# Kernel optimization log

Measured on AMD Instinct MI355X. Metric: run time of the kernel, lower is better.

## Reference

```python
import jax, jax.numpy as jnp
import numpy as np

SEGMENT_LENGTHS = (768, 1536, 3072, 6144, 12288)
DILATED_RATIOS = (1, 2, 4, 8, 16)
NUM_HEADS = 12
NEG_INF = -1e9


def _layer_norm(x, g, b, eps=1e-5):
    mu = jnp.mean(x, axis=-1, keepdims=True)
    var = jnp.mean((x - mu) ** 2, axis=-1, keepdims=True)
    return (x - mu) * jax.lax.rsqrt(var + eps) * g + b


def _dilated_branch(q, k, v, w, r):
    # q,k,v: (B, L, H, Dh); segment length w, dilation ratio r (w % r == 0)
    B, L, H, Dh = q.shape
    Lp = -(-L // w) * w
    n, m = Lp // w, w // r
    gsz = -(-H // r)  # head-group size (heads padded up to a multiple of r in LongNet)
    offs = jnp.arange(H) // gsz  # per-head token offset within each r-block
    oh = jax.nn.one_hot(offs, r, dtype=q.dtype)  # (H, r)

    def gather(t):
        t = jnp.pad(t, ((0, 0), (0, Lp - L), (0, 0), (0, 0)))
        t = t.reshape(B, n, m, r, H, Dh)  # segments of w = m blocks of r
        return jnp.einsum('bnmrhd,hr->bnmhd', t, oh)  # each head picks its offset

    qi, ki, vi = gather(q), gather(k), gather(v)
    s = jnp.einsum('bnihd,bnjhd->bnhij', qi * (Dh ** -0.5), ki)  # (B,n,H,m,m)
    lse = jax.scipy.special.logsumexp(s, axis=-1)  # (B,n,H,m)
    o = jnp.einsum('bnhij,bnjhd->bnihd', jax.nn.softmax(s, axis=-1), vi)
    # scatter back to dense token positions; uncovered slots get 0 / -inf lse
    o_full = jnp.einsum('bnmhd,hr->bnmrhd', o, oh).reshape(B, Lp, H, Dh)
    lse = jnp.transpose(lse, (0, 1, 3, 2))  # (B,n,m,H)
    lse_full = jnp.where(oh.T[None, None, None] > 0, lse[:, :, :, None, :], NEG_INF)
    lse_full = lse_full.reshape(B, Lp, H)
    return o_full[:, :L], lse_full[:, :L]


def _dilated_attention(q, k, v):
    outs, lses = [], []
    for w, r in zip(SEGMENT_LENGTHS, DILATED_RATIOS):
        o, l = _dilated_branch(q, k, v, w, r)
        outs.append(o)
        lses.append(l)
    lse = jnp.stack(lses)  # (n_branch, B, L, H)
    wts = jnp.exp(lse - lse.max(0))
    wts = wts / wts.sum(0)  # softmax-combine branches by their lse (LongNet recombination)
    return (jnp.stack(outs) * wts[..., None]).sum(0)  # (B, L, H, Dh)


def _forward(x, patch_w, patch_b, cls_token, pos_embed,
             ln1_g, ln1_b, wq, bq, wk, bk, wv, bv, wo, bo,
             ln2_g, ln2_b, w1, b1, w2, b2, normf_g, normf_b, head_w, head_b):
    B, Cin, D, Hs, Ws = x.shape
    E = patch_w.shape[0]
    pd, ph, pw = patch_w.shape[2], patch_w.shape[3], patch_w.shape[4]
    # non-overlapping 3D patch embed (Conv3d with stride == kernel)
    xp = x.reshape(B, Cin, D // pd, pd, Hs // ph, ph, Ws // pw, pw)
    tok = jnp.einsum('bcxpyqzr,ecpqr->bxyze', xp, patch_w).reshape(B, -1, E) + patch_b
    tok = tok + pos_embed[:, 1:]
    cls = cls_token + pos_embed[:, :1]
    h = jnp.concatenate([jnp.broadcast_to(cls, (B, 1, E)), tok], axis=1)
    L = h.shape[1]
    Dh = E // NUM_HEADS
    depth = wq.shape[0]
    for i in range(depth):  # pre-LN transformer layers with LongNet dilated attention
        hn = _layer_norm(h, ln1_g[i], ln1_b[i])
        q = (hn @ wq[i] + bq[i]).reshape(B, L, NUM_HEADS, Dh)
        k = (hn @ wk[i] + bk[i]).reshape(B, L, NUM_HEADS, Dh)
        v = (hn @ wv[i] + bv[i]).reshape(B, L, NUM_HEADS, Dh)
        a = _dilated_attention(q, k, v).reshape(B, L, E)
        h = h + a @ wo[i] + bo[i]
        hn = _layer_norm(h, ln2_g[i], ln2_b[i])
        h = h + jax.nn.gelu(hn @ w1[i] + b1[i], approximate=False) @ w2[i] + b2[i]
    h = _layer_norm(h, normf_g, normf_b)
    return h[:, 0] @ head_w + head_b  # (B, num_classes)


def setup_inputs() -> dict:
    key = jax.random.key(0)
    ks = jax.random.split(key, 12)
    B, E, depth, ncls = 2, 768, 2, 1000
    D, Hs, Ws = 48, 256, 256
    N = (D // 4) * (Hs // 16) * (Ws // 16)  # 3072 patches
    f32 = jnp.float32
    s = 0.02
    return {
        'x': jax.random.normal(ks[0], (B, 1, D, Hs, Ws), f32),
        'patch_w': jax.random.normal(ks[1], (E, 1, 4, 16, 16), f32) * s,
        'patch_b': jnp.zeros((E,), f32),
        'cls_token': jax.random.normal(ks[2], (1, 1, E), f32) * s,
        'pos_embed': jax.random.normal(ks[3], (1, N + 1, E), f32) * s,
        'ln1_g': jnp.ones((depth, E), f32),
        'ln1_b': jnp.zeros((depth, E), f32),
        'wq': jax.random.normal(ks[4], (depth, E, E), f32) * s,
        'bq': jnp.zeros((depth, E), f32),
        'wk': jax.random.normal(ks[5], (depth, E, E), f32) * s,
        'bk': jnp.zeros((depth, E), f32),
        'wv': jax.random.normal(ks[6], (depth, E, E), f32) * s,
        'bv': jnp.zeros((depth, E), f32),
        'wo': jax.random.normal(ks[7], (depth, E, E), f32) * s,
        'bo': jnp.zeros((depth, E), f32),
        'ln2_g': jnp.ones((depth, E), f32),
        'ln2_b': jnp.zeros((depth, E), f32),
        'w1': jax.random.normal(ks[8], (depth, E, 4 * E), f32) * s,
        'b1': jnp.zeros((depth, 4 * E), f32),
        'w2': jax.random.normal(ks[9], (depth, 4 * E, E), f32) * s,
        'b2': jnp.zeros((depth, E), f32),
        'normf_g': jnp.ones((E,), f32),
        'normf_b': jnp.zeros((E,), f32),
        'head_w': jax.random.normal(ks[10], (E, ncls), f32) * s,
        'head_b': jnp.zeros((ncls,), f32),
    }


def reference(x, patch_w, patch_b, cls_token, pos_embed,
              ln1_g, ln1_b, wq, bq, wk, bk, wv, bv, wo, bo,
              ln2_g, ln2_b, w1, b1, w2, b2, normf_g, normf_b, head_w, head_b):
    return _forward(x, patch_w, patch_b, cls_token, pos_embed,
                    ln1_g, ln1_b, wq, bq, wk, bk, wv, bv, wo, bo,
                    ln2_g, ln2_b, w1, b1, w2, b2, normf_g, normf_b, head_w, head_b)
```

## Files before the change

kernel.cpp:

```cpp
#include <hip/hip_runtime.h>
#include <math.h>

#define TOK_L 3073
#define EMB 768
#define NH 12
#define DH 64
#define BATCH 2
#define QKVS 2304
#define HSZ ((size_t)BATCH * TOK_L * EMB)
#define MHC ((size_t)BATCH * TOK_L * NH)

typedef __bf16 bf16;
typedef __bf16 v8bf __attribute__((ext_vector_type(8)));
typedef __bf16 v4bf __attribute__((ext_vector_type(4)));
typedef float  v4f  __attribute__((ext_vector_type(4)));
typedef unsigned int v4u __attribute__((ext_vector_type(4)));

__device__ __forceinline__ v8bf zero8() {
    v8bf v;
    #pragma unroll
    for (int i = 0; i < 8; i++) v[i] = (bf16)0.f;
    return v;
}
__device__ __forceinline__ v4f zero4() {
    v4f v; v[0] = 0.f; v[1] = 0.f; v[2] = 0.f; v[3] = 0.f; return v;
}
__device__ __forceinline__ float gelu_f(float x) {
    return 0.5f * x * (1.0f + erff(x * 0.70710678118654752f));
}
__device__ __forceinline__ void gload16(const bf16* g, bf16* l) {
    __builtin_amdgcn_global_load_lds(
        (const __attribute__((address_space(1))) void*)g,
        (__attribute__((address_space(3))) void*)l, 16, 0, 0);
}
__device__ __forceinline__ v8bf lds_read128(const bf16* p) {
    v8bf r;
    asm volatile("ds_read_b128 %0, %1"
        : "=v"(r)
        : "v"((const __attribute__((address_space(3))) bf16*)p));
    return r;
}

__device__ __forceinline__ void convT_tile(const float* __restrict__ src,
                                           bf16* __restrict__ dst,
                                           int K, int N, int tx, int ty)
{
    __shared__ float t[32][33];
    int n0 = tx * 32, k0 = ty * 32;
    int r = threadIdx.x >> 3, c4 = (threadIdx.x & 7) * 4;
    float4 v = *(const float4*)(src + (size_t)(k0 + r) * N + n0 + c4);
    t[r][c4 + 0] = v.x; t[r][c4 + 1] = v.y; t[r][c4 + 2] = v.z; t[r][c4 + 3] = v.w;
    __syncthreads();
    v4bf o;
    o[0] = (bf16)t[c4 + 0][r]; o[1] = (bf16)t[c4 + 1][r];
    o[2] = (bf16)t[c4 + 2][r]; o[3] = (bf16)t[c4 + 3][r];
    *(v4bf*)(dst + (size_t)(n0 + r) * K + k0 + c4) = o;
}

__global__ __launch_bounds__(256) void prep_weights(
    const float* __restrict__ wq, const float* __restrict__ wk,
    const float* __restrict__ wv, const float* __restrict__ wo,
    const float* __restrict__ w1, const float* __restrict__ w2,
    const float* __restrict__ patch_w,
    bf16* __restrict__ qkv_t0, bf16* __restrict__ wo_t0,
    bf16* __restrict__ w1_t, bf16* __restrict__ w2_t, bf16* __restrict__ pw_b)
{
    int bid = blockIdx.x;
    if (bid >= 13824) {
        int i = ((bid - 13824) * 256 + threadIdx.x) * 4;
        float4 v = *(const float4*)(patch_w + i);
        v4bf o; o[0] = (bf16)v.x; o[1] = (bf16)v.y; o[2] = (bf16)v.z; o[3] = (bf16)v.w;
        *(v4bf*)(pw_b + i) = o;
        return;
    }
    int layer = bid / 6912, t = bid % 6912;
    if (t < 1728) {
        int m = t / 576, tt = t % 576;
        const float* src = (m == 0 ? wq : m == 1 ? wk : wv) + (size_t)layer * 589824;
        bf16* dst = qkv_t0 + (size_t)layer * QKVS * 768 + (size_t)m * 589824;
        convT_tile(src, dst, 768, 768, tt % 24, tt / 24);
    } else if (t < 2304) {
        int tt = t - 1728;
        convT_tile(wo + (size_t)layer * 589824, wo_t0 + (size_t)layer * 589824,
                   768, 768, tt % 24, tt / 24);
    } else if (t < 4608) {
        int tt = t - 2304;
        convT_tile(w1 + (size_t)layer * 2359296, w1_t + (size_t)layer * 2359296,
                   768, 3072, tt % 96, tt / 96);
    } else {
        int tt = t - 4608;
        convT_tile(w2 + (size_t)layer * 2359296, w2_t + (size_t)layer * 2359296,
                   3072, 768, tt % 24, tt / 24);
    }
}

__global__ __launch_bounds__(256) void prep_small(const float* __restrict__ bq,
    const float* __restrict__ bk, const float* __restrict__ bv, float* __restrict__ d,
    const float* __restrict__ cls, const float* __restrict__ pos, float* __restrict__ h)
{
    int i = blockIdx.x * 256 + threadIdx.x;
    if (i < 2 * QKVS) {
        int layer = i / QKVS, j = i % QKVS;
        const float* s = (j < 768) ? bq : (j < 1536) ? bk : bv;
        d[i] = s[(size_t)layer * 768 + (j & 767)];
    }
    if (i < 2 * 768) {
        int b = i / 768, e = i % 768;
        h[(size_t)b * TOK_L * EMB + e] = cls[e] + pos[e];
    }
}

__global__ __launch_bounds__(256) void gather_patches(const float* __restrict__ x,
                                                      bf16* __restrict__ Xp) {
    int p = blockIdx.x;
    int b = p / 3072, pp = p % 3072;
    int px = pp >> 8, py = (pp >> 4) & 15, pz = pp & 15;
    for (int k = threadIdx.x; k < 1024; k += 256) {
        int pd = k >> 8, ph = (k >> 4) & 15, pw = k & 15;
        size_t src = ((size_t)(b * 48 + px * 4 + pd)) * 65536
                   + (size_t)(py * 16 + ph) * 256 + (size_t)(pz * 16 + pw);
        Xp[(size_t)p * 1024 + k] = (bf16)x[src];
    }
}

__device__ __forceinline__ void remap_tile(int NX, int MY, int G, int& xo, int& yo)
{
    int id = blockIdx.x + NX * blockIdx.y;
    int nwg = NX * MY;
    int xcd = id & 7, j = id >> 3;
    int q = nwg >> 3, r = nwg & 7;
    int n = xcd * q + (xcd < r ? xcd : r) + j;
    int full = MY / G;
    int bpg = NX * G;
    int nf = full * bpg;
    if (n < nf) {
        int gi = n / bpg, w = n - gi * bpg;
        int xi = w / G;
        xo = xi; yo = gi * G + (w - xi * G);
    } else {
        int t = MY - full * G;
        int w = n - nf;
        int xi = w / t;
        xo = xi; yo = full * G + (w - xi * t);
    }
}

__global__ __launch_bounds__(512, 2) void gemm256(
    const bf16* __restrict__ A, const bf16* __restrict__ Bt,
    const float* __restrict__ bias, bf16* __restrict__ Cb,
    int M, int N, int K, int dogelu, int G)
{
    __shared__ bf16 AB[65536];
    const int tid = threadIdx.x;
    const int lane = tid & 63, wid = tid >> 6;
    const int ln15 = lane & 15, q4 = lane >> 4;
    int xo, yo;
    remap_tile(gridDim.x, gridDim.y, G, xo, yo);
    const int m0 = yo * 256, n0 = xo * 256;
    const int wm = (wid & 1) * 128, wn = (wid >> 1) * 64;
    const int srow = wid * 8 + (lane >> 3);
    const int schunk = ((lane & 7) ^ ((lane >> 3) & 7)) * 8;
    const int NT = K >> 6;

    auto stageA = [&](int t, int h) {
        const int slot = (2 * t + h) & 3;
        bf16* dstb = AB + slot * 8192 + wid * 512;
        const int k0 = t << 6;
        #pragma unroll
        for (int i = 0; i < 2; i++) {
            int gm = m0 + h * 128 + i * 64 + srow; if (gm >= M) gm = M - 1;
            gload16(A + (size_t)gm * K + k0 + schunk, dstb + i * 4096);
        }
    };
    auto stageB = [&](int t, int h) {
        const int slot = (2 * t + h) & 3;
        bf16* dstb = AB + 32768 + slot * 8192 + wid * 512;
        const int k0 = t << 6;
        #pragma unroll
        for (int i = 0; i < 2; i++) {
            int gn = n0 + h * 128 + i * 64 + srow;
            gload16(Bt + (size_t)gn * K + k0 + schunk, dstb + i * 4096);
        }
    };
    auto rdA = [&](int kt, int mt, int ks) -> v8bf {
        int R = wm + mt * 16 + ln15;
        int slot = (2 * kt + (R >> 7)) & 3;
        int r7 = R & 127;
        return lds_read128(AB + slot * 8192 + r7 * 64 + ((ks * 4 + q4) ^ (r7 & 7)) * 8);
    };
    auto rdB = [&](int kt, int nt, int ks) -> v8bf {
        int C = wn + nt * 16 + ln15;
        int slot = (2 * kt + (C >> 7)) & 3;
        int c7 = C & 127;
        return lds_read128(AB + 32768 + slot * 8192 + c7 * 64 + ((ks * 4 + q4) ^ (c7 & 7)) * 8);
    };

    v4f acc[8][4];
    #pragma unroll
    for (int i = 0; i < 8; i++)
        #pragma unroll
        for (int j = 0; j < 4; j++) acc[i][j] = zero4();

    stageA(0, 0); stageA(0, 1); stageB(0, 0); stageB(0, 1);
    if (NT > 1) { stageA(1, 0); stageA(1, 1); }

    v8bf af[8][2], bfr[4][2];
    for (int kt = 0; kt < NT; kt++) {
        if (kt + 1 < NT) {
            stageB(kt + 1, 0);
            asm volatile("s_waitcnt vmcnt(6)" ::: "memory");
        } else {
            asm volatile("s_waitcnt vmcnt(0)" ::: "memory");
        }
        __builtin_amdgcn_sched_barrier(0);
        __builtin_amdgcn_s_barrier();
        __builtin_amdgcn_sched_barrier(0);
        #pragma unroll
        for (int mt = 0; mt < 4; mt++) { af[mt][0] = rdA(kt, mt, 0); af[mt][1] = rdA(kt, mt, 1); }
        #pragma unroll
        for (int nt = 0; nt < 2; nt++) { bfr[nt][0] = rdB(kt, nt, 0); bfr[nt][1] = rdB(kt, nt, 1); }
        asm volatile("s_waitcnt lgkmcnt(0)" ::: "memory");
        __builtin_amdgcn_sched_barrier(0);
        __builtin_amdgcn_s_setprio(1);
        #pragma unroll
        for (int mt = 0; mt < 4; mt++)
            #pragma unroll
            for (int nt = 0; nt < 2; nt++)
                #pragma unroll
                for (int ks = 0; ks < 2; ks++)
                    acc[mt][nt] = __builtin_amdgcn_mfma_f32_16x16x32_bf16(af[mt][ks], bfr[nt][ks], acc[mt][nt], 0, 0, 0);
        __builtin_amdgcn_s_setprio(0);
        __builtin_amdgcn_s_barrier();
        #pragma unroll
        for (int mt = 4; mt < 8; mt++) { af[mt][0] = rdA(kt, mt, 0); af[mt][1] = rdA(kt, mt, 1); }
        #pragma unroll
        for (int nt = 2; nt < 4; nt++) { bfr[nt][0] = rdB(kt, nt, 0); bfr[nt][1] = rdB(kt, nt, 1); }
        if (kt + 1 < NT) stageB(kt + 1, 1);
        __builtin_amdgcn_s_barrier();
        asm volatile("s_waitcnt lgkmcnt(0)" ::: "memory");
        __builtin_amdgcn_sched_barrier(0);
        __builtin_amdgcn_s_setprio(1);
        #pragma unroll
        for (int mt = 0; mt < 4; mt++)
            #pragma unroll
            for (int nt = 2; nt < 4; nt++)
                #pragma unroll
                for (int ks = 0; ks < 2; ks++)
                    acc[mt][nt] = __builtin_amdgcn_mfma_f32_16x16x32_bf16(af[mt][ks], bfr[nt][ks], acc[mt][nt], 0, 0, 0);
        __builtin_amdgcn_s_setprio(0);
        __builtin_amdgcn_s_barrier();
        if (kt + 2 < NT) stageA(kt + 2, 0);
        __builtin_amdgcn_s_barrier();
        __builtin_amdgcn_sched_barrier(0);
        __builtin_amdgcn_s_setprio(1);
        #pragma unroll
        for (int mt = 4; mt < 8; mt++)
            #pragma unroll
            for (int nt = 2; nt < 4; nt++)
                #pragma unroll
                for (int ks = 0; ks < 2; ks++)
                    acc[mt][nt] = __builtin_amdgcn_mfma_f32_16x16x32_bf16(af[mt][ks], bfr[nt][ks], acc[mt][nt], 0, 0, 0);
        __builtin_amdgcn_s_setprio(0);
        __builtin_amdgcn_s_barrier();
        if (kt + 2 < NT) stageA(kt + 2, 1);
        __builtin_amdgcn_s_barrier();
        __builtin_amdgcn_sched_barrier(0);
        __builtin_amdgcn_s_setprio(1);
        #pragma unroll
        for (int mt = 4; mt < 8; mt++)
            #pragma unroll
            for (int nt = 0; nt < 2; nt++)
                #pragma unroll
                for (int ks = 0; ks < 2; ks++)
                    acc[mt][nt] = __builtin_amdgcn_mfma_f32_16x16x32_bf16(af[mt][ks], bfr[nt][ks], acc[mt][nt], 0, 0, 0);
        __builtin_amdgcn_s_setprio(0);
        __builtin_amdgcn_s_barrier();
    }

    #pragma unroll
    for (int mt = 0; mt < 8; mt++) {
        #pragma unroll
        for (int nt = 0; nt < 4; nt++) {
            #pragma unroll
            for (int g = 0; g < 4; g++) {
                int row = m0 + wm + mt * 16 + q4 * 4 + g;
                if (row >= M) continue;
                int col = n0 + wn + nt * 16 + ln15;
                float v = acc[mt][nt][g] + bias[col];
                if (dogelu) v = gelu_f(v);
                Cb[(size_t)row * N + col] = (bf16)v;
            }
        }
    }
}

template<int BN>
__global__ __launch_bounds__(256) void gemm_bf16(
    const bf16* __restrict__ A, const bf16* __restrict__ Bt,
    const float* __restrict__ bias, float* __restrict__ Cf,
    bf16* __restrict__ Cb, int M, int N, int K, int flags,
    const float* __restrict__ pos, int G)
{
    __shared__ bf16 As[3][128 * 32];
    __shared__ bf16 Bs[3][BN * 32];
    const int tid = threadIdx.x;
    const int lane = tid & 63, wid = tid >> 6;
    const int ln15 = lane & 15, q4 = lane >> 4;
    int xo, yo;
    remap_tile(gridDim.x, gridDim.y, G, xo, yo);
    const int m0 = yo * 128, n0 = xo * BN;
    const int wm = (wid & 1) * 64, wn = (wid >> 1) * (BN / 2);
    const int srow = lane >> 2;
    const int schunk = (lane & 3) * 8;
    const int NF = BN / 32;

    v4f acc[4][NF];
    #pragma unroll
    for (int i = 0; i < 4; i++)
        #pragma unroll
        for (int j = 0; j < NF; j++) acc[i][j] = zero4();

    const int NT = K >> 5;
    auto stage = [&](int kt, int bi) {
        const int k0 = kt << 5;
        #pragma unroll
        for (int i = 0; i < 2; i++) {
            int rg = wid * 32 + i * 16;
            int gm = m0 + rg + srow; if (gm >= M) gm = M - 1;
            gload16(A + (size_t)gm * K + k0 + schunk, &As[bi][rg * 32]);
        }
        if (BN == 128) {
            #pragma unroll
            for (int i = 0; i < 2; i++) {
                int rg = wid * 32 + i * 16;
                gload16(Bt + (size_t)(n0 + rg + srow) * K + k0 + schunk, &Bs[bi][rg * 32]);
            }
        } else {
            int rg = wid * 16;
            gload16(Bt + (size_t)(n0 + rg + srow) * K + k0 + schunk, &Bs[bi][rg * 32]);
        }
    };

    stage(0, 0);
    if (NT > 1) stage(1, 1);

    int cur = 0;
    for (int kt = 0; kt < NT; kt++) {
        int nx2 = cur + 2; if (nx2 >= 3) nx2 -= 3;
        if (kt + 2 < NT) {
            stage(kt + 2, nx2);
            if (BN == 128) asm volatile("s_waitcnt vmcnt(8)" ::: "memory");
            else           asm volatile("s_waitcnt vmcnt(6)" ::: "memory");
        } else if (kt + 1 < NT) {
            if (BN == 128) asm volatile("s_waitcnt vmcnt(4)" ::: "memory");
            else           asm volatile("s_waitcnt vmcnt(3)" ::: "memory");
        } else {
            asm volatile("s_waitcnt vmcnt(0)" ::: "memory");
        }
        __builtin_amdgcn_sched_barrier(0);
        __builtin_amdgcn_s_barrier();

        v8bf af[4], bfr[NF];
        #pragma unroll
        for (int mt = 0; mt < 4; mt++)
            af[mt] = *(const v8bf*)(&As[cur][(wm + mt * 16 + ln15) * 32 + q4 * 8]);
        #pragma unroll
        for (int nt = 0; nt < NF; nt++)
            bfr[nt] = *(const v8bf*)(&Bs[cur][(wn + nt * 16 + ln15) * 32 + q4 * 8]);
        #pragma unroll
        for (int mt = 0; mt < 4; mt++)
            #pragma unroll
            for (int nt = 0; nt < NF; nt++)
                acc[mt][nt] = __builtin_amdgcn_mfma_f32_16x16x32_bf16(af[mt], bfr[nt], acc[mt][nt], 0, 0, 0);
        __builtin_amdgcn_s_barrier();
        cur = cur + 1 == 3 ? 0 : cur + 1;
    }
    #pragma unroll
    for (int mt = 0; mt < 4; mt++) {
        #pragma unroll
        for (int nt = 0; nt < NF; nt++) {
            #pragma unroll
            for (int g = 0; g < 4; g++) {
                int row = m0 + wm + mt * 16 + q4 * 4 + g;
                if (row >= M) continue;
                int col = n0 + wn + nt * 16 + ln15;
                float v = acc[mt][nt][g] + bias[col];
                if (flags & 2) v = gelu_f(v);
                size_t crow;
                if (flags & 4) {
                    int rowp = row % 3072;
                    crow = (size_t)(row + row / 3072 + 1);
                    v += pos[(size_t)(rowp + 1) * EMB + col];
                } else crow = (size_t)row;
                size_t ci = crow * (size_t)N + col;
                if (flags & 8) Cb[ci] = (bf16)v;
                else { if (flags & 1) v += Cf[ci]; Cf[ci] = v; }
            }
        }
    }
}

__global__ __launch_bounds__(256) void layernorm_kernel(
    const float* __restrict__ x, const float* __restrict__ g,
    const float* __restrict__ bb, bf16* __restrict__ y, int nrows)
{
    int row = blockIdx.x;
    if (row >= nrows) return;
    int tid = threadIdx.x;
    const float* xr = x + (size_t)row * EMB;
    float v0 = xr[tid], v1 = xr[tid + 256], v2 = xr[tid + 512];
    __shared__ float red[256];
    red[tid] = v0 + v1 + v2;
    __syncthreads();
    for (int o = 128; o > 0; o >>= 1) { if (tid < o) red[tid] += red[tid + o]; __syncthreads(); }
    float mu = red[0] * (1.f / 768.f);
    __syncthreads();
    float d0 = v0 - mu, d1 = v1 - mu, d2 = v2 - mu;
    red[tid] = d0 * d0 + d1 * d1 + d2 * d2;
    __syncthreads();
    for (int o = 128; o > 0; o >>= 1) { if (tid < o) red[tid] += red[tid + o]; __syncthreads(); }
    float rs = rsqrtf(red[0] * (1.f / 768.f) + 1e-5f);
    bf16* yr = y + (size_t)row * EMB;
    yr[tid]       = (bf16)(d0 * rs * g[tid]       + bb[tid]);
    yr[tid + 256] = (bf16)(d1 * rs * g[tid + 256] + bb[tid + 256]);
    yr[tid + 512] = (bf16)(d2 * rs * g[tid + 512] + bb[tid + 512]);
}

__global__ __launch_bounds__(256) void pack_vt(const bf16* __restrict__ qkv,
                                               bf16* __restrict__ Vt)
{
    __shared__ bf16 t[64 * 65];
    int yy = blockIdx.y;
    int br, seg;
    if (yy < 5)       { br = 0; seg = yy; }
    else if (yy < 8)  { br = 1; seg = yy - 5; }
    else if (yy < 10) { br = 2; seg = yy - 8; }
    else if (yy == 10){ br = 3; seg = 0; }
    else              { br = 4; seg = 0; }
    const int r = 1 << br, w = 768 << br;
    const int gsz = (NH + r - 1) / r;
    const int bh = blockIdx.z;
    const int b = bh / NH, hd = bh % NH;
    const int off = hd / gsz;
    const int kbase = seg * w + off;
    const int kt = blockIdx.x;
    const int tid = threadIdx.x;
    const int dq = (tid & 7) * 8;
    #pragma unroll
    for (int p = 0; p < 2; p++) {
        int jl = (tid >> 3) + p * 32;
        int pk = kbase + (kt * 64 + jl) * r;
        v8bf val = (pk < TOK_L)
            ? *(const v8bf*)(qkv + (size_t)(b * TOK_L + pk) * QKVS + 1536 + hd * DH + dq)
            : zero8();
        #pragma unroll
        for (int i = 0; i < 8; i++) t[jl * 65 + dq + i] = val[i];
    }
    __syncthreads();
    #pragma unroll
    for (int p = 0; p < 2; p++) {
        int d = (tid >> 3) + p * 32;
        int kk = (tid & 7) * 8;
        v8bf o;
        #pragma unroll
        for (int i = 0; i < 8; i++) o[i] = t[(kk + i) * 65 + d];
        *(v8bf*)(Vt + ((size_t)(yy * 24 + bh) * 64 + d) * 768 + kt * 64 + kk) = o;
    }
}

__global__ __launch_bounds__(256) void attn_mfma(
    const bf16* __restrict__ qkv, const bf16* __restrict__ Vt,
    bf16* __restrict__ oac, bf16* __restrict__ obr, float* __restrict__ lse5)
{
    __shared__ bf16 kl[2 * 4096];
    const int tid = threadIdx.x;
    const int lane = tid & 63, wid = tid >> 6;
    const int ln15 = lane & 15, q4 = lane >> 4;
    const int bid = blockIdx.x;
    const int xcd = bid & 7, rest = bid >> 3;
    const int slot = rest / 6, t = rest - slot * 6;
    const int g = (slot << 3) | xcd;
    const int yy = g / 24, bh = g - yy * 24;
    int br, seg;
    if (yy < 5)       { br = 0; seg = yy; }
    else if (yy < 8)  { br = 1; seg = yy - 5; }
    else if (yy < 10) { br = 2; seg = yy - 8; }
    else if (yy == 10){ br = 3; seg = 0; }
    else              { br = 4; seg = 0; }
    const int r = 1 << br, w = 768 << br;
    const int gsz = (NH + r - 1) / r;
    const int b = bh / NH, hd = bh % NH;
    const int off = hd / gsz;
    const int sbase = seg * w + off;
    if (sbase + (t * 128) * r >= TOK_L) return;

    int n_valid = (TOK_L - sbase + r - 1) / r;
    if (n_valid > 768) n_valid = 768;
    const int kt_lim = (n_valid + 63) >> 6;
    const float pad_add = (float)(768 - n_valid);
    const int qoff = t * 128 + wid * 32;
    const bool wactive = (sbase + qoff * r) < TOK_L;

    const bf16* qb_ = qkv + hd * DH;
    const bf16* kb_ = qkv + 768 + hd * DH;

    const int swz = (ln15 & 7) * 8;

    auto stageK = [&](int ktv, int bufi) {
        #pragma unroll
        for (int p = 0; p < 2; p++) {
            int row = (tid >> 3) + p * 32;
            int pk = sbase + (ktv * 64 + row) * r;
            if (pk >= TOK_L) pk = 0;
            int colsw = ((tid & 7) ^ ((tid >> 3) & 7)) * 8;
            gload16(kb_ + (size_t)(b * TOK_L + pk) * QKVS + colsw,
                    kl + bufi * 4096 + wid * 512 + p * 2048);
        }
    };

    v8bf qf[2][2];
    #pragma unroll
    for (int mt = 0; mt < 2; mt++) {
        int pq = sbase + (qoff + mt * 16 + ln15) * r;
        #pragma unroll
        for (int ks = 0; ks < 2; ks++) {
            v8bf qv = (pq < TOK_L)
                ? *(const v8bf*)(qb_ + (size_t)(b * TOK_L + pq) * QKVS + ks * 32 + q4 * 8)
                : zero8();
            #pragma unroll
            for (int i = 0; i < 8; i++) qv[i] = (bf16)((float)qv[i] * 0.125f);
            qf[mt][ks] = qv;
        }
    }
    v4f o[2][4];
    float lsum[2];
    #pragma unroll
    for (int mt = 0; mt < 2; mt++) {
        lsum[mt] = 0.f;
        #pragma unroll
        for (int dt = 0; dt < 4; dt++) o[mt][dt] = zero4();
    }

    const bf16* vtb = Vt + (size_t)(yy * 24 + bh) * 64 * 768;

    stageK(0, 0);
    __syncthreads();

    for (int kt = 0; kt < kt_lim; kt++) {
        const int cur = kt & 1;
        if (kt + 1 < kt_lim) stageK(kt + 1, cur ^ 1);
        if (wactive) {
            const bf16* klc = kl + cur * 4096;
            v8bf kf[4][2];
            #pragma unroll
            for (int nt = 0; nt < 4; nt++)
                #pragma unroll
                for (int ks = 0; ks < 2; ks++)
                    kf[nt][ks] = *(const v8bf*)(klc + (nt * 16 + ln15) * 64
                                                + ((ks * 32 + q4 * 8) ^ swz));
            unsigned int paw[2][2][4];
            #pragma unroll
            for (int mt = 0; mt < 2; mt++) {
                v4f s[4];
                #pragma unroll
                for (int nt = 0; nt < 4; nt++) {
                    s[nt] = __builtin_amdgcn_mfma_f32_16x16x32_bf16(kf[nt][0], qf[mt][0], zero4(), 0, 0, 0);
                    s[nt] = __builtin_amdgcn_mfma_f32_16x16x32_bf16(kf[nt][1], qf[mt][1], s[nt], 0, 0, 0);
                }
                unsigned int W[4][2];
                float ls = 0.f;
                #pragma unroll
                for (int nt = 0; nt < 4; nt++) {
                    int kb = kt * 64 + nt * 16 + q4 * 4;
                    float p0 = (kb + 0 < n_valid) ? __expf(s[nt][0]) : 0.f;
                    float p1 = (kb + 1 < n_valid) ? __expf(s[nt][1]) : 0.f;
                    float p2 = (kb + 2 < n_valid) ? __expf(s[nt][2]) : 0.f;
                    float p3 = (kb + 3 < n_valid) ? __expf(s[nt][3]) : 0.f;
                    ls += (p0 + p1) + (p2 + p3);
                    asm("v_cvt_pk_bf16_f32 %0, %1, %2" : "=v"(W[nt][0]) : "v"(p0), "v"(p1));
                    asm("v_cvt_pk_bf16_f32 %0, %1, %2" : "=v"(W[nt][1]) : "v"(p2), "v"(p3));
                }
                lsum[mt] += ls;
                #pragma unroll
                for (int ks = 0; ks < 2; ks++) {
                    #pragma unroll
                    for (int h = 0; h < 2; h++) {
                        unsigned int a = W[2 * ks][h], c = W[2 * ks + 1][h];
                        asm("v_permlane32_swap_b32 %0, %1" : "+v"(a), "+v"(c));
                        asm("v_permlane16_swap_b32 %0, %1" : "+v"(a), "+v"(c));
                        paw[mt][ks][h]     = a;
                        paw[mt][ks][2 + h] = c;
                    }
                }
            }
            #pragma unroll
            for (int ks = 0; ks < 2; ks++) {
                v8bf vf[4];
                #pragma unroll
                for (int dt = 0; dt < 4; dt++)
                    vf[dt] = *(const v8bf*)(vtb + (size_t)(dt * 16 + ln15) * 768 + kt * 64 + ks * 32 + q4 * 8);
                #pragma unroll
                for (int mt = 0; mt < 2; mt++) {
                    v4u pw = { paw[mt][ks][0], paw[mt][ks][1], paw[mt][ks][2], paw[mt][ks][3] };
                    v8bf pa = __builtin_bit_cast(v8bf, pw);
                    #pragma unroll
                    for (int dt = 0; dt < 4; dt++)
                        o[mt][dt] = __builtin_amdgcn_mfma_f32_16x16x32_bf16(pa, vf[dt], o[mt][dt], 0, 0, 0);
                }
            }
        }
        __syncthreads();
    }
    if (!wactive) return;

    float lf[2];
    #pragma unroll
    for (int mt = 0; mt < 2; mt++) {
        float l = lsum[mt];
        l += __shfl_xor(l, 16, 64);
        l += __shfl_xor(l, 32, 64);
        l += pad_add;
        lf[mt] = l;
        if (q4 == 0) {
            int pq = sbase + (qoff + mt * 16 + ln15) * r;
            if (pq < TOK_L)
                lse5[(size_t)br * MHC + (size_t)(b * TOK_L + pq) * NH + hd] = __logf(l);
        }
    }

    bf16* od = (br == 0) ? oac : obr + (size_t)(br - 1) * HSZ;
    #pragma unroll
    for (int mt = 0; mt < 2; mt++) {
        #pragma unroll
        for (int g2 = 0; g2 < 4; g2++) {
            float l = __shfl(lf[mt], q4 * 4 + g2, 64);
            int row = mt * 16 + q4 * 4 + g2;
            int pq = sbase + (qoff + row) * r;
            if (pq >= TOK_L) continue;
            float linv = 1.f / l;
            #pragma unroll
            for (int dt = 0; dt < 4; dt++)
                od[(size_t)(b * TOK_L + pq) * EMB + hd * DH + dt * 16 + ln15] =
                    (bf16)(o[mt][dt][g2] * linv);
        }
    }
}

__global__ __launch_bounds__(256) void attn_combine(
    const bf16* __restrict__ oac, const bf16* __restrict__ obr,
    const float* __restrict__ lse5, bf16* __restrict__ outb)
{
    size_t e = (size_t)blockIdx.x * 256 + threadIdx.x;
    if (e >= HSZ) return;
    size_t g = e >> 6;
    int h = (int)(g % NH);
    int p = (int)((g / NH) % TOK_L);
    float l0 = lse5[g];
    float m = l0;
    float lv[4];
    bool cov[4];
    #pragma unroll
    for (int j = 0; j < 4; j++) {
        int r = 2 << j;
        int gsz = (NH + r - 1) / r;
        cov[j] = ((p & (r - 1)) == (h / gsz));
        if (cov[j]) {
            lv[j] = lse5[(size_t)(j + 1) * MHC + g];
            m = fmaxf(m, lv[j]);
        }
    }
    float w0 = __expf(l0 - m);
    float wsum = w0;
    float acc = w0 * (float)oac[e];
    #pragma unroll
    for (int j = 0; j < 4; j++) {
        if (cov[j]) {
            float wj = __expf(lv[j] - m);
            wsum += wj;
            acc = fmaf(wj, (float)obr[(size_t)j * HSZ + e], acc);
        }
    }
    outb[e] = (bf16)(acc / wsum);
}

__global__ __launch_bounds__(256) void head_kernel(
    const bf16* __restrict__ hn, const float* __restrict__ hw,
    const float* __restrict__ hb, float* __restrict__ out)
{
    int b = blockIdx.y;
    int c = blockIdx.x * 256 + threadIdx.x;
    __shared__ float srow[EMB];
    for (int e = threadIdx.x; e < EMB; e += 256)
        srow[e] = (float)hn[(size_t)b * TOK_L * EMB + e];
    __syncthreads();
    if (c < 1000) {
        float acc = hb[c];
        for (int e = 0; e < EMB; e++)
            acc = fmaf(srow[e], hw[(size_t)e * 1000 + c], acc);
        out[b * 1000 + c] = acc;
    }
}

extern "C" void kernel_launch(void* const* d_in, const int* in_sizes, int n_in,
                              void* d_out, int out_size, void* d_ws, size_t ws_size,
                              hipStream_t stream)
{
    const float* x       = (const float*)d_in[0];
    const float* patch_w = (const float*)d_in[1];
    const float* patch_b = (const float*)d_in[2];
    const float* cls_tok = (const float*)d_in[3];
    const float* pos_emb = (const float*)d_in[4];
    const float* ln1_g   = (const float*)d_in[5];
    const float* ln1_b   = (const float*)d_in[6];
    const float* wq      = (const float*)d_in[7];
    const float* bq      = (const float*)d_in[8];
    const float* wk      = (const float*)d_in[9];
    const float* bk      = (const float*)d_in[10];
    const float* wv      = (const float*)d_in[11];
    const float* bv      = (const float*)d_in[12];
    const float* wo      = (const float*)d_in[13];
    const float* bo      = (const float*)d_in[14];
    const float* ln2_g   = (const float*)d_in[15];
    const float* ln2_b   = (const float*)d_in[16];
    const float* w1      = (const float*)d_in[17];
    const float* b1      = (const float*)d_in[18];
    const float* w2      = (const float*)d_in[19];
    const float* b2      = (const float*)d_in[20];
    const float* normf_g = (const float*)d_in[21];
    const float* normf_b = (const float*)d_in[22];
    const float* head_w  = (const float*)d_in[23];
    const float* head_b  = (const float*)d_in[24];
    float* out = (float*)d_out;

    char* wp = (char*)d_ws;
    auto alloc = [&](size_t bytes) { char* r = wp; wp += (bytes + 255) & ~(size_t)255; return r; };
    float* h    = (float*)alloc(HSZ * 4);
    bf16*  hn   = (bf16*)alloc(HSZ * 2);
    bf16*  QKV  = (bf16*)alloc((size_t)BATCH * TOK_L * QKVS * 2);
    bf16*  oac  = (bf16*)alloc(HSZ * 2);
    float* lse5 = (float*)alloc(5 * MHC * 4);
    bf16*  Vt   = (bf16*)alloc((size_t)12 * 24 * 64 * 768 * 2);
    bf16*  mid  = (bf16*)alloc(4 * HSZ * 2);
    bf16*  obr  = mid;
    bf16*  Xp   = mid;

    bf16*  qkv_t0 = (bf16*)alloc((size_t)2 * QKVS * 768 * 2);
    bf16*  wo_t0  = (bf16*)alloc((size_t)2 * 768 * 768 * 2);
    bf16*  w1_t   = (bf16*)alloc((size_t)2 * 3072 * 768 * 2);
    bf16*  w2_t   = (bf16*)alloc((size_t)2 * 768 * 3072 * 2);
    bf16*  pw_b   = (bf16*)alloc((size_t)768 * 1024 * 2);
    float* bqkv   = (float*)alloc((size_t)2 * QKVS * 4);

    const int M = BATCH * TOK_L;
    const int MT = (M + 127) / 128;
    const int MT2 = (M + 255) / 256;

    prep_weights<<<dim3(14592), 256, 0, stream>>>(wq, wk, wv, wo, w1, w2, patch_w,
                                                  qkv_t0, wo_t0, w1_t, w2_t, pw_b);
    prep_small<<<dim3(18), 256, 0, stream>>>(bq, bk, bv, bqkv, cls_tok, pos_emb, h);

    gather_patches<<<dim3(BATCH * 3072), 256, 0, stream>>>(x, Xp);
    gemm_bf16<64><<<dim3(12, 48), 256, 0, stream>>>(Xp, pw_b, patch_b, h, nullptr,
                                                    BATCH * 3072, 768, 1024, 4, pos_emb, 8);

    for (int layer = 0; layer < 2; layer++) {
        size_t bOff  = (size_t)layer * 768;
        size_t b1Off = (size_t)layer * 3072;
        bf16* qt   = qkv_t0 + (size_t)layer * QKVS * 768;
        bf16* wo_t = wo_t0 + (size_t)layer * 589824;

        layernorm_kernel<<<dim3(M), 256, 0, stream>>>(h, ln1_g + bOff, ln1_b + bOff, hn, M);
        gemm256<<<dim3(9, MT2), 512, 0, stream>>>(hn, qt, bqkv + (size_t)layer * QKVS,
                                                  QKV, M, QKVS, 768, 0, 4);

        pack_vt<<<dim3(12, 12, 24), 256, 0, stream>>>(QKV, Vt);
        attn_mfma<<<dim3(1728), 256, 0, stream>>>(QKV, Vt, oac, obr, lse5);
        attn_combine<<<dim3((unsigned)((HSZ + 255) / 256)), 256, 0, stream>>>(oac, obr, lse5, hn);

        gemm_bf16<64><<<dim3(12, MT), 256, 0, stream>>>(hn, wo_t, bo + bOff, h, nullptr,
                                                        M, 768, 768, 1, nullptr, 8);

        layernorm_kernel<<<dim3(M), 256, 0, stream>>>(h, ln2_g + bOff, ln2_b + bOff, hn, M);
        gemm256<<<dim3(12, MT2), 512, 0, stream>>>(hn, w1_t + (size_t)layer * 2359296, b1 + b1Off,
                                                   mid, M, 3072, 768, 1, 4);
        gemm_bf16<64><<<dim3(12, MT), 256, 0, stream>>>(mid, w2_t + (size_t)layer * 2359296, b2 + bOff,
                                                        h, nullptr, M, 768, 3072, 1, nullptr, 4);
    }

    layernorm_kernel<<<dim3(M), 256, 0, stream>>>(h, normf_g, normf_b, hn, M);
    head_kernel<<<dim3(4, BATCH), 256, 0, stream>>>(hn, head_w, head_b, out);
}
```

Measured before the change: 998.4 us.

## Restage gemm256 loads, vectorize gather/combine, warp-shuffle layernorm, swap QKV GEMM

Reorders the gemm256 main loop so each quarter-step reloads its own A/B fragments into smaller register arrays and prefetches only the next k-tile, which lowers register pressure but shortens the prefetch distance. Separately, the patch gather and attention-combine kernels now use vectorized float4/bf16x2 accesses, and layernorm uses wave shuffles instead of a shared-memory tree reduction. The QKV projection moves from gemm256 to gemm_bf16<128> with a different grid and flags. These are several independent local changes bundled together.

```diff
diff --git a/kernel.cpp b/kernel.cpp
--- a/kernel.cpp
+++ b/kernel.cpp
@@ -13,6 +13,7 @@
 typedef __bf16 bf16;
 typedef __bf16 v8bf __attribute__((ext_vector_type(8)));
 typedef __bf16 v4bf __attribute__((ext_vector_type(4)));
+typedef __bf16 v2bf __attribute__((ext_vector_type(2)));
 typedef float  v4f  __attribute__((ext_vector_type(4)));
 typedef unsigned int v4u __attribute__((ext_vector_type(4)));
 
@@ -115,12 +116,13 @@
     int p = blockIdx.x;
     int b = p / 3072, pp = p % 3072;
     int px = pp >> 8, py = (pp >> 4) & 15, pz = pp & 15;
-    for (int k = threadIdx.x; k < 1024; k += 256) {
-        int pd = k >> 8, ph = (k >> 4) & 15, pw = k & 15;
-        size_t src = ((size_t)(b * 48 + px * 4 + pd)) * 65536
-                   + (size_t)(py * 16 + ph) * 256 + (size_t)(pz * 16 + pw);
-        Xp[(size_t)p * 1024 + k] = (bf16)x[src];
-    }
+    int k = threadIdx.x * 4;
+    int pd = k >> 8, ph = (k >> 4) & 15, pw = k & 15;
+    size_t src = ((size_t)(b * 48 + px * 4 + pd)) * 65536
+               + (size_t)(py * 16 + ph) * 256 + (size_t)(pz * 16 + pw);
+    float4 v = *(const float4*)(x + src);
+    v4bf o; o[0] = (bf16)v.x; o[1] = (bf16)v.y; o[2] = (bf16)v.z; o[3] = (bf16)v.w;
+    *(v4bf*)(Xp + (size_t)p * 1024 + k) = o;
 }
 
 __device__ __forceinline__ void remap_tile(int NX, int MY, int G, int& xo, int& yo)
@@ -202,78 +204,98 @@
         for (int j = 0; j < 4; j++) acc[i][j] = zero4();
 
     stageA(0, 0); stageA(0, 1); stageB(0, 0); stageB(0, 1);
-    if (NT > 1) { stageA(1, 0); stageA(1, 1); }
-
-    v8bf af[8][2], bfr[4][2];
+
     for (int kt = 0; kt < NT; kt++) {
         if (kt + 1 < NT) {
-            stageB(kt + 1, 0);
-            asm volatile("s_waitcnt vmcnt(6)" ::: "memory");
+            stageA(kt + 1, 0);
+            asm volatile("s_waitcnt vmcnt(2)" ::: "memory");
         } else {
             asm volatile("s_waitcnt vmcnt(0)" ::: "memory");
         }
         __builtin_amdgcn_sched_barrier(0);
         __builtin_amdgcn_s_barrier();
         __builtin_amdgcn_sched_barrier(0);
-        #pragma unroll
-        for (int mt = 0; mt < 4; mt++) { af[mt][0] = rdA(kt, mt, 0); af[mt][1] = rdA(kt, mt, 1); }
-        #pragma unroll
-        for (int nt = 0; nt < 2; nt++) { bfr[nt][0] = rdB(kt, nt, 0); bfr[nt][1] = rdB(kt, nt, 1); }
-        asm volatile("s_waitcnt lgkmcnt(0)" ::: "memory");
-        __builtin_amdgcn_sched_barrier(0);
-        __builtin_amdgcn_s_setprio(1);
-        #pragma unroll
-        for (int mt = 0; mt < 4; mt++)
-            #pragma unroll
-            for (int nt = 0; nt < 2; nt++)
-                #pragma unroll
-                for (int ks = 0; ks < 2; ks++)
-                    acc[mt][nt] = __builtin_amdgcn_mfma_f32_16x16x32_bf16(af[mt][ks], bfr[nt][ks], acc[mt][nt], 0, 0, 0);
-        __builtin_amdgcn_s_setprio(0);
+        {
+            v8bf af[4][2], bfr[2][2];
+            #pragma unroll
+            for (int mt = 0; mt < 4; mt++) { af[mt][0] = rdA(kt, mt, 0); af[mt][1] = rdA(kt, mt, 1); }
+            #pragma unroll
+            for (int nt = 0; nt < 2; nt++) { bfr[nt][0] = rdB(kt, nt, 0); bfr[nt][1] = rdB(kt, nt, 1); }
+            asm volatile("s_waitcnt lgkmcnt(0)" ::: "memory");
+            __builtin_amdgcn_sched_barrier(0);
+            __builtin_amdgcn_s_setprio(1);
+            #pragma unroll
+            for (int mt = 0; mt < 4; mt++)
+                #pragma unroll
+                for (int nt = 0; nt < 2; nt++)
+                    #pragma unroll
+                    for (int ks = 0; ks < 2; ks++)
+                        acc[mt][nt] = __builtin_amdgcn_mfma_f32_16x16x32_bf16(af[mt][ks], bfr[nt][ks], acc[mt][nt], 0, 0, 0);
+            __builtin_amdgcn_s_setprio(0);
+        }
         __builtin_amdgcn_s_barrier();
-        #pragma unroll
-        for (int mt = 4; mt < 8; mt++) { af[mt][0] = rdA(kt, mt, 0); af[mt][1] = rdA(kt, mt, 1); }
-        #pragma unroll
-        for (int nt = 2; nt < 4; nt++) { bfr[nt][0] = rdB(kt, nt, 0); bfr[nt][1] = rdB(kt, nt, 1); }
-        if (kt + 1 < NT) stageB(kt + 1, 1);
+        {
+            v8bf af[4][2], bfr[2][2];
+            #pragma unroll
+            for (int mt = 0; mt < 4; mt++) { af[mt][0] = rdA(kt, mt, 0); af[mt][1] = rdA(kt, mt, 1); }
+            #pragma unroll
+            for (int nt = 0; nt < 2; nt++) { bfr[nt][0] = rdB(kt, nt + 2, 0); bfr[nt][1] = rdB(kt, nt + 2, 1); }
+            if (kt + 1 < NT) stageA(kt + 1, 1);
+            __builtin_amdgcn_s_barrier();
+            asm volatile("s_waitcnt lgkmcnt(0)" ::: "memory");
+            __builtin_amdgcn_sched_barrier(0);
+            __builtin_amdgcn_s_setprio(1);
+            #pragma unroll
+            for (int mt = 0; mt < 4; mt++)
+                #pragma unroll
+                for (int nt = 0; nt < 2; nt++)
+                    #pragma unroll
+                    for (int ks = 0; ks < 2; ks++)
+                        acc[mt][nt + 2] = __builtin_amdgcn_mfma_f32_16x16x32_bf16(af[mt][ks], bfr[nt][ks], acc[mt][nt + 2], 0, 0, 0);
+            __builtin_amdgcn_s_setprio(0);
+        }
         __builtin_amdgcn_s_barrier();
-        asm volatile("s_waitcnt lgkmcnt(0)" ::: "memory");
-        __builtin_amdgcn_sched_barrier(0);
-        __builtin_amdgcn_s_setprio(1);
-        #pragma unroll
-        for (int mt = 0; mt < 4; mt++)
-            #pragma unroll
-            for (int nt = 2; nt < 4; nt++)
-                #pragma unroll
-                for (int ks = 0; ks < 2; ks++)
-                    acc[mt][nt] = __builtin_amdgcn_mfma_f32_16x16x32_bf16(af[mt][ks], bfr[nt][ks], acc[mt][nt], 0, 0, 0);
-        __builtin_amdgcn_s_setprio(0);
+        {
+            v8bf af[4][2], bfr[2][2];
+            #pragma unroll
+            for (int mt = 0; mt < 4; mt++) { af[mt][0] = rdA(kt, mt + 4, 0); af[mt][1] = rdA(kt, mt + 4, 1); }
+            #pragma unroll
+            for (int nt = 0; nt < 2; nt++) { bfr[nt][0] = rdB(kt, nt, 0); bfr[nt][1] = rdB(kt, nt, 1); }
+            if (kt + 1 < NT) stageB(kt + 1, 0);
+            __builtin_amdgcn_s_barrier();
+            asm volatile("s_waitcnt lgkmcnt(0)" ::: "memory");
+            __builtin_amdgcn_sched_barrier(0);
+            __builtin_amdgcn_s_setprio(1);
+            #pragma unroll
+            for (int mt = 0; mt < 4; mt++)
+                #pragma unroll
+                for (int nt = 0; nt < 2; nt++)
+                    #pragma unroll
+                    for (int ks = 0; ks < 2; ks++)
+                        acc[mt + 4][nt] = __builtin_amdgcn_mfma_f32_16x16x32_bf16(af[mt][ks], bfr[nt][ks], acc[mt + 4][nt], 0, 0, 0);
+            __builtin_amdgcn_s_setprio(0);
+        }
         __builtin_amdgcn_s_barrier();
-        if (kt + 2 < NT) stageA(kt + 2, 0);
-        __builtin_amdgcn_s_barrier();
-        __builtin_amdgcn_sched_barrier(0);
-        __builtin_amdgcn_s_setprio(1);
-        #pragma unroll
-        for (int mt = 4; mt < 8; mt++)
-            #pragma unroll
-            for (int nt = 2; nt < 4; nt++)
-                #pragma unroll
-                for (int ks = 0; ks < 2; ks++)
-                    acc[mt][nt] = __builtin_amdgcn_mfma_f32_16x16x32_bf16(af[mt][ks], bfr[nt][ks], acc[mt][nt], 0, 0, 0);
-        __builtin_amdgcn_s_setprio(0);
-        __builtin_amdgcn_s_barrier();
-        if (kt + 2 < NT) stageA(kt + 2, 1);
-        __builtin_amdgcn_s_barrier();
-        __builtin_amdgcn_sched_barrier(0);
-        __builtin_amdgcn_s_setprio(1);
-        #pragma unroll
-        for (int mt = 4; mt < 8; mt++)
-            #pragma unroll
-            for (int nt = 0; nt < 2; nt++)
-                #pragma unroll
-                for (int ks = 0; ks < 2; ks++)
-                    acc[mt][nt] = __builtin_amdgcn_mfma_f32_16x16x32_bf16(af[mt][ks], bfr[nt][ks], acc[mt][nt], 0, 0, 0);
-        __builtin_amdgcn_s_setprio(0);
+        {
+            v8bf af[4][2], bfr[2][2];
+            #pragma unroll
+            for (int mt = 0; mt < 4; mt++) { af[mt][0] = rdA(kt, mt + 4, 0); af[mt][1] = rdA(kt, mt + 4, 1); }
+            #pragma unroll
+            for (int nt = 0; nt < 2; nt++) { bfr[nt][0] = rdB(kt, nt + 2, 0); bfr[nt][1] = rdB(kt, nt + 2, 1); }
+            if (kt + 1 < NT) stageB(kt + 1, 1);
+            __builtin_amdgcn_s_barrier();
+            asm volatile("s_waitcnt lgkmcnt(0)" ::: "memory");
+            __builtin_amdgcn_sched_barrier(0);
+            __builtin_amdgcn_s_setprio(1);
+            #pragma unroll
+            for (int mt = 0; mt < 4; mt++)
+                #pragma unroll
+                for (int nt = 0; nt < 2; nt++)
+                    #pragma unroll
+                    for (int ks = 0; ks < 2; ks++)
+                        acc[mt + 4][nt + 2] = __builtin_amdgcn_mfma_f32_16x16x32_bf16(af[mt][ks], bfr[nt][ks], acc[mt + 4][nt + 2], 0, 0, 0);
+            __builtin_amdgcn_s_setprio(0);
+        }
         __builtin_amdgcn_s_barrier();
     }
 
@@ -407,19 +429,24 @@
     int row = blockIdx.x;
     if (row >= nrows) return;
     int tid = threadIdx.x;
+    int lane = tid & 63, wv = tid >> 6;
     const float* xr = x + (size_t)row * EMB;
     float v0 = xr[tid], v1 = xr[tid + 256], v2 = xr[tid + 512];
-    __shared__ float red[256];
-    red[tid] = v0 + v1 + v2;
+    __shared__ float ws[4], ws2[4];
+    float s = v0 + v1 + v2;
+    #pragma unroll
+    for (int o = 1; o < 64; o <<= 1) s += __shfl_xor(s, o, 64);
+    if (lane == 0) ws[wv] = s;
     __syncthreads();
-    for (int o = 128; o > 0; o >>= 1) { if (tid < o) red[tid] += red[tid + o]; __syncthreads(); }
-    float mu = red[0] * (1.f / 768.f);
+    float mu = (ws[0] + ws[1] + ws[2] + ws[3]) * (1.f / 768.f);
+    float d0 = v0 - mu, d1 = v1 - mu, d2 = v2 - mu;
+    float q = d0 * d0 + d1 * d1 + d2 * d2;
+    #pragma unroll
+    for (int o = 1; o < 64; o <<= 1) q += __shfl_xor(q, o, 64);
+    if (lane == 0) ws2[wv] = q;
     __syncthreads();
-    float d0 = v0 - mu, d1 = v1 - mu, d2 = v2 - mu;
-    red[tid] = d0 * d0 + d1 * d1 + d2 * d2;
-    __syncthreads();
-    for (int o = 128; o > 0; o >>= 1) { if (tid < o) red[tid] += red[tid + o]; __syncthreads(); }
-    float rs = rsqrtf(red[0] * (1.f / 768.f) + 1e-5f);
+    float var = (ws2[0] + ws2[1] + ws2[2] + ws2[3]) * (1.f / 768.f);
+    float rs = rsqrtf(var + 1e-5f);
     bf16* yr = y + (size_t)row * EMB;
     yr[tid]       = (bf16)(d0 * rs * g[tid]       + bb[tid]);
     yr[tid + 256] = (bf16)(d1 * rs * g[tid + 256] + bb[tid + 256]);
@@ -650,7 +677,7 @@
     const bf16* __restrict__ oac, const bf16* __restrict__ obr,
     const float* __restrict__ lse5, bf16* __restrict__ outb)
 {
-    size_t e = (size_t)blockIdx.x * 256 + threadIdx.x;
+    size_t e = ((size_t)blockIdx.x * 256 + threadIdx.x) * 2;
     if (e >= HSZ) return;
     size_t g = e >> 6;
     int h = (int)(g % NH);
@@ -671,16 +698,22 @@
     }
     float w0 = __expf(l0 - m);
     float wsum = w0;
-    float acc = w0 * (float)oac[e];
+    v2bf a0 = *(const v2bf*)(oac + e);
+    float acc0 = w0 * (float)a0[0];
+    float acc1 = w0 * (float)a0[1];
     #pragma unroll
     for (int j = 0; j < 4; j++) {
         if (cov[j]) {
             float wj = __expf(lv[j] - m);
             wsum += wj;
-            acc = fmaf(wj, (float)obr[(size_t)j * HSZ + e], acc);
-        }
-    }
-    outb[e] = (bf16)(acc / wsum);
+            v2bf aj = *(const v2bf*)(obr + (size_t)j * HSZ + e);
+            acc0 = fmaf(wj, (float)aj[0], acc0);
+            acc1 = fmaf(wj, (float)aj[1], acc1);
+        }
+    }
+    float inv = 1.f / wsum;
+    v2bf o2; o2[0] = (bf16)(acc0 * inv); o2[1] = (bf16)(acc1 * inv);
+    *(v2bf*)(outb + e) = o2;
 }
 
 __global__ __launch_bounds__(256) void head_kernel(
@@ -770,12 +803,12 @@
         bf16* wo_t = wo_t0 + (size_t)layer * 589824;
 
         layernorm_kernel<<<dim3(M), 256, 0, stream>>>(h, ln1_g + bOff, ln1_b + bOff, hn, M);
-        gemm256<<<dim3(9, MT2), 512, 0, stream>>>(hn, qt, bqkv + (size_t)layer * QKVS,
-                                                  QKV, M, QKVS, 768, 0, 4);
+        gemm_bf16<128><<<dim3(18, MT), 256, 0, stream>>>(hn, qt, bqkv + (size_t)layer * QKVS,
+                                                         nullptr, QKV, M, QKVS, 768, 8, nullptr, 8);
 
         pack_vt<<<dim3(12, 12, 24), 256, 0, stream>>>(QKV, Vt);
         attn_mfma<<<dim3(1728), 256, 0, stream>>>(QKV, Vt, oac, obr, lse5);
-        attn_combine<<<dim3((unsigned)((HSZ + 255) / 256)), 256, 0, stream>>>(oac, obr, lse5, hn);
+        attn_combine<<<dim3((unsigned)((HSZ / 2 + 255) / 256)), 256, 0, stream>>>(oac, obr, lse5, hn);
 
         gemm_bf16<64><<<dim3(12, MT), 256, 0, stream>>>(hn, wo_t, bo + bOff, h, nullptr,
                                                         M, 768, 768, 1, nullptr, 8);
```

New measurement: 1.017 ms. No clear change (+1.8%).
